# Kernel tuning notes

Measured on AMD Instinct MI355X. Metric: run time of the kernel, lower is better.

The kernel has to match this reference:

```python
import jax, jax.numpy as jnp
import numpy as np

N_NODES = 50000
BN_EPS = 1e-5


def setup_inputs() -> dict:
    key = jax.random.key(0)
    ks = jax.random.split(key, 6)
    N, E, CIN, CH, COUT = N_NODES, 800000, 128, 256, 128
    node_feat = jax.random.normal(ks[0], (N, CIN), dtype=jnp.float32)
    edge_index = jax.random.randint(ks[1], (2, E), 0, N, dtype=jnp.int64)
    # Glorot-ish init for weights
    W1 = jax.random.normal(ks[2], (CIN, CH), dtype=jnp.float32) / np.sqrt(CIN)
    b1 = jnp.zeros((CH,), dtype=jnp.float32)
    bn_gamma = jnp.ones((CH,), dtype=jnp.float32)
    bn_beta = jnp.zeros((CH,), dtype=jnp.float32)
    W2 = jax.random.normal(ks[3], (CH, COUT), dtype=jnp.float32) / np.sqrt(CH)
    b2 = jnp.zeros((COUT,), dtype=jnp.float32)
    return {"node_feat": node_feat, "edge_index": edge_index, "W1": W1, "b1": b1,
            "bn_gamma": bn_gamma, "bn_beta": bn_beta, "W2": W2, "b2": b2}


def gcn_conv(x, W, b, src, dst, n_nodes):
    """PyG GCNConv: out = D^-1/2 (A+I) D^-1/2 (x W) + b."""
    h = x @ W                                   # [N, C_out]
    loop = jnp.arange(n_nodes, dtype=src.dtype)
    src_f = jnp.concatenate([src, loop])        # self-loops appended
    dst_f = jnp.concatenate([dst, loop])
    deg = jax.ops.segment_sum(jnp.ones_like(dst_f, dtype=h.dtype), dst_f,
                              num_segments=n_nodes)
    dinv = jax.lax.rsqrt(jnp.maximum(deg, 1.0))  # deg >= 1 due to self-loops
    norm = dinv[src_f] * dinv[dst_f]             # [E+N]
    msg = h[src_f] * norm[:, None]               # gather + scale
    return jax.ops.segment_sum(msg, dst_f, num_segments=n_nodes) + b


def batch_norm(x, gamma, beta):
    mean = jnp.mean(x, axis=0)
    var = jnp.mean((x - mean) ** 2, axis=0)      # biased var (torch BN normalization)
    return (x - mean) * jax.lax.rsqrt(var + BN_EPS) * gamma + beta


def reference(node_feat, edge_index, W1, b1, bn_gamma, bn_beta, W2, b2):
    src, dst = edge_index[0], edge_index[1]
    x = gcn_conv(node_feat, W1, b1, src, dst, N_NODES)
    x = batch_norm(x, bn_gamma, bn_beta)
    x = jax.nn.relu(x)
    # dropout is identity at inference
    x = gcn_conv(x, W2, b2, src, dst, N_NODES)
    return x
```

## Files before the change

### kernel.cpp

```cpp
#include <hip/hip_runtime.h>
#include <hip/hip_fp16.h>

#define CIN 128
#define CH 256
#define COUT 128
#define BN_EPS 1e-5f

typedef __attribute__((ext_vector_type(8))) short bf16x8;
typedef __attribute__((ext_vector_type(4))) float f32x4;

__device__ __forceinline__ short f2bf(float x) {
    unsigned u = __float_as_uint(x);
    unsigned r = (u + 0x7fffu + ((u >> 16) & 1u)) >> 16;
    return (short)r;
}
__device__ __forceinline__ float bf2f(short h) {
    return __uint_as_float(((unsigned)(unsigned short)h) << 16);
}

__global__ void k_deg(const int* __restrict__ dst, int* __restrict__ degi,
                      unsigned short* __restrict__ rank, int E) {
    int e = blockIdx.x * 256 + threadIdx.x;
    if (e < E) rank[e] = (unsigned short)atomicAdd(&degi[dst[e]], 1);
}

__global__ void k_scan1(const int* __restrict__ degi, float* __restrict__ dinv,
                        int* __restrict__ blocksum, int N) {
    __shared__ int s[256];
    int i = blockIdx.x * 256 + threadIdx.x;
    int v = (i < N) ? degi[i] : 0;
    if (i < N) dinv[i] = rsqrtf((float)(v + 1));
    s[threadIdx.x] = v;
    __syncthreads();
    for (int st = 128; st > 0; st >>= 1) {
        if (threadIdx.x < st) s[threadIdx.x] += s[threadIdx.x + st];
        __syncthreads();
    }
    if (threadIdx.x == 0) blocksum[blockIdx.x] = s[0];
}

__global__ void k_scan3(const int* __restrict__ degi, const int* __restrict__ blocksum,
                        int nb, int* __restrict__ rowstart, int N, int E) {
    __shared__ int sb[256];
    __shared__ int s[256];
    int bv = (threadIdx.x < nb) ? blocksum[threadIdx.x] : 0;
    sb[threadIdx.x] = bv;
    __syncthreads();
    for (int st = 1; st < 256; st <<= 1) {
        int t = (threadIdx.x >= st) ? sb[threadIdx.x - st] : 0;
        __syncthreads();
        sb[threadIdx.x] += t;
        __syncthreads();
    }
    int boff = (blockIdx.x == 0) ? 0 : sb[blockIdx.x - 1];

    int i = blockIdx.x * 256 + threadIdx.x;
    int v = (i < N) ? degi[i] : 0;
    s[threadIdx.x] = v;
    __syncthreads();
    for (int st = 1; st < 256; st <<= 1) {
        int t = (threadIdx.x >= st) ? s[threadIdx.x - st] : 0;
        __syncthreads();
        s[threadIdx.x] += t;
        __syncthreads();
    }
    if (i < N) rowstart[i] = s[threadIdx.x] - v + boff;
    if (blockIdx.x == 0 && threadIdx.x == 0) rowstart[N] = E;
}

__global__ void k_fill(const int* __restrict__ src, const int* __restrict__ dst,
                       const unsigned short* __restrict__ rank,
                       const int* __restrict__ rowstart,
                       unsigned short* __restrict__ csr, int E) {
    int e = blockIdx.x * 256 + threadIdx.x;
    if (e >= E) return;
    int d = dst[e];
    int pos = rowstart[d] + (int)rank[e];
    __builtin_nontemporal_store((unsigned short)src[e], &csr[pos]);
}

__global__ void k_prep(const float* __restrict__ W1, const float* __restrict__ W2,
                       short* __restrict__ W1sw, short* __restrict__ W2sw,
                       const float4* __restrict__ nf, short4* __restrict__ nfb, int n4) {
    int t = blockIdx.x * 256 + threadIdx.x;
    if (t < 32768) {
        int n = t >> 7, kk = t & 127;
        float v = W1[kk * 256 + n];
        short h = f2bf(v);
        short l = f2bf(v - bf2f(h));
        int t16 = n >> 4, m = n & 15;
        int ks = kk >> 5, q = (kk >> 3) & 3, j = kk & 7;
        int idx = (t16 * 4 + ks) * 1024 + (q * 16 + m) * 8 + j;
        W1sw[idx] = h;
        W1sw[idx + 512] = l;
    } else if (t < 65536) {
        int u = t - 32768;
        int n = u >> 8, kk = u & 255;
        float v = W2[kk * 128 + n];
        short h = f2bf(v);
        short l = f2bf(v - bf2f(h));
        int t16 = n >> 4, m = n & 15;
        int ks = kk >> 5, q = (kk >> 3) & 3, j = kk & 7;
        int idx = (t16 * 8 + ks) * 1024 + (q * 16 + m) * 8 + j;
        W2sw[idx] = h;
        W2sw[idx + 512] = l;
    } else {
        int u = t - 65536;
        if (u < n4) {
            float4 v = nf[u];
            short4 s;
            s.x = f2bf(v.x); s.y = f2bf(v.y); s.z = f2bf(v.z); s.w = f2bf(v.w);
            nfb[u] = s;
        }
    }
}

template <int MODE>
__global__ __launch_bounds__(256) void k_gather(const short* __restrict__ xb,
                                                const int* __restrict__ rowstart,
                                                const unsigned short* __restrict__ csr,
                                                const float* __restrict__ dinv,
                                                const float* __restrict__ bias,
                                                float* __restrict__ out,
                                                short* __restrict__ ob, int N) {
    int t = blockIdx.x * 256 + threadIdx.x;
    int r = t >> 4;
    int c = t & 15;
    if (r >= N) return;
    float di = dinv[r];
    float w0 = di * di;
    bf16x8 sv = *(const bf16x8*)(xb + (size_t)r * 128 + c * 8);
    float acc[8];
    #pragma unroll
    for (int j = 0; j < 8; ++j) acc[j] = bf2f(sv[j]) * w0;
    int e0 = rowstart[r], e1 = rowstart[r + 1];
    int e = e0;
    for (; e + 7 < e1; e += 8) {
        int s[8];
        #pragma unroll
        for (int i = 0; i < 8; ++i) s[i] = csr[e + i];
        float w[8];
        #pragma unroll
        for (int i = 0; i < 8; ++i) w[i] = dinv[s[i]] * di;
        bf16x8 x[8];
        #pragma unroll
        for (int i = 0; i < 8; ++i) x[i] = *(const bf16x8*)(xb + (size_t)s[i] * 128 + c * 8);
        #pragma unroll
        for (int i = 0; i < 8; ++i)
            #pragma unroll
            for (int j = 0; j < 8; ++j) acc[j] = fmaf(w[i], bf2f(x[i][j]), acc[j]);
    }
    for (; e + 3 < e1; e += 4) {
        int s[4];
        #pragma unroll
        for (int i = 0; i < 4; ++i) s[i] = csr[e + i];
        float w[4];
        #pragma unroll
        for (int i = 0; i < 4; ++i) w[i] = dinv[s[i]] * di;
        bf16x8 x[4];
        #pragma unroll
        for (int i = 0; i < 4; ++i) x[i] = *(const bf16x8*)(xb + (size_t)s[i] * 128 + c * 8);
        #pragma unroll
        for (int i = 0; i < 4; ++i)
            #pragma unroll
            for (int j = 0; j < 8; ++j) acc[j] = fmaf(w[i], bf2f(x[i][j]), acc[j]);
    }
    for (; e < e1; ++e) {
        int s0 = csr[e];
        float ww = dinv[s0] * di;
        bf16x8 x0 = *(const bf16x8*)(xb + (size_t)s0 * 128 + c * 8);
        #pragma unroll
        for (int j = 0; j < 8; ++j) acc[j] = fmaf(ww, bf2f(x0[j]), acc[j]);
    }
    if (MODE == 0) {
        bf16x8 h;
        #pragma unroll
        for (int j = 0; j < 8; ++j) h[j] = f2bf(acc[j]);
        *(bf16x8*)(ob + (size_t)r * 128 + c * 8) = h;
    } else {
        float4 b0 = *(const float4*)(bias + c * 8);
        float4 b1 = *(const float4*)(bias + c * 8 + 4);
        float4 o0 = make_float4(acc[0] + b0.x, acc[1] + b0.y, acc[2] + b0.z, acc[3] + b0.w);
        float4 o1 = make_float4(acc[4] + b1.x, acc[5] + b1.y, acc[6] + b1.z, acc[7] + b1.w);
        *(float4*)(out + (size_t)r * 128 + c * 8) = o0;
        *(float4*)(out + (size_t)r * 128 + c * 8 + 4) = o1;
    }
}

__device__ __forceinline__ bf16x8 bnrelu8(bf16x8 raw, const float* __restrict__ scsh, int c) {
    float4 sc0 = *(const float4*)(scsh + c);
    float4 sc1 = *(const float4*)(scsh + c + 4);
    float4 sh0 = *(const float4*)(scsh + 256 + c);
    float4 sh1 = *(const float4*)(scsh + 256 + c + 4);
    bf16x8 o;
    o[0] = f2bf(fmaxf(fmaf(bf2f(raw[0]), sc0.x, sh0.x), 0.f));
    o[1] = f2bf(fmaxf(fmaf(bf2f(raw[1]), sc0.y, sh0.y), 0.f));
    o[2] = f2bf(fmaxf(fmaf(bf2f(raw[2]), sc0.z, sh0.z), 0.f));
    o[3] = f2bf(fmaxf(fmaf(bf2f(raw[3]), sc0.w, sh0.w), 0.f));
    o[4] = f2bf(fmaxf(fmaf(bf2f(raw[4]), sc1.x, sh1.x), 0.f));
    o[5] = f2bf(fmaxf(fmaf(bf2f(raw[5]), sc1.y, sh1.y), 0.f));
    o[6] = f2bf(fmaxf(fmaf(bf2f(raw[6]), sc1.z, sh1.z), 0.f));
    o[7] = f2bf(fmaxf(fmaf(bf2f(raw[7]), sc1.w, sh1.w), 0.f));
    return o;
}

template <int K, int NOUT, bool STATS, bool BIAS, bool BNRELU>
__global__ __launch_bounds__(256, 2) void k_gemm(const short* __restrict__ A,
                                                 const short* __restrict__ Bsw,
                                                 const float* __restrict__ bias,
                                                 const float* __restrict__ scsh,
                                                 short* __restrict__ C,
                                                 float* __restrict__ stats, int M) {
    constexpr int CT = NOUT / 64;
    constexpr int KS = K / 32;
    constexpr int KP = K + 8;
    constexpr int LROW = NOUT + 8;
    constexpr int LSZ = (64 * KP > 64 * LROW) ? 64 * KP : 64 * LROW;
    __shared__ __align__(16) short lds[LSZ];
    int tid = threadIdx.x;
    int wave = tid >> 6;
    int lane = tid & 63;
    int m = lane & 15;
    int q = lane >> 4;
    int row0 = blockIdx.x * 64;

    constexpr int CPRA = K / 8;
    #pragma unroll
    for (int i = 0; i < (64 * CPRA) / 256; ++i) {
        int idx = i * 256 + tid;
        int r = idx / CPRA, cc = idx % CPRA;
        int gr = row0 + r;
        if (gr >= M) gr = M - 1;
        bf16x8 v = *(const bf16x8*)(A + (size_t)gr * K + cc * 8);
        if (BNRELU) v = bnrelu8(v, scsh, cc * 8);
        *(bf16x8*)(lds + r * KP + cc * 8) = v;
    }
    __syncthreads();

    f32x4 acc[4][CT];
    #pragma unroll
    for (int rt = 0; rt < 4; ++rt)
        #pragma unroll
        for (int ct = 0; ct < CT; ++ct)
            acc[rt][ct] = (f32x4){0.f, 0.f, 0.f, 0.f};

    #pragma unroll
    for (int ks = 0; ks < KS; ++ks) {
        bf16x8 bh[CT], bl[CT];
        #pragma unroll
        for (int ct = 0; ct < CT; ++ct) {
            const short* bp = Bsw + (size_t)((wave * CT + ct) * KS + ks) * 1024 + lane * 8;
            bh[ct] = *(const bf16x8*)bp;
            bl[ct] = *(const bf16x8*)(bp + 512);
        }
        bf16x8 af[4];
        #pragma unroll
        for (int rt = 0; rt < 4; ++rt)
            af[rt] = *(const bf16x8*)(lds + (rt * 16 + m) * KP + ks * 32 + q * 8);
        #pragma unroll
        for (int ct = 0; ct < CT; ++ct)
            #pragma unroll
            for (int rt = 0; rt < 4; ++rt) {
                acc[rt][ct] = __builtin_amdgcn_mfma_f32_16x16x32_bf16(af[rt], bh[ct], acc[rt][ct], 0, 0, 0);
                acc[rt][ct] = __builtin_amdgcn_mfma_f32_16x16x32_bf16(af[rt], bl[ct], acc[rt][ct], 0, 0, 0);
            }
    }
    __syncthreads();

    #pragma unroll
    for (int ct = 0; ct < CT; ++ct) {
        int col = wave * (NOUT / 4) + ct * 16 + m;
        float bv = BIAS ? bias[col] : 0.f;
        float s = 0.f, sq = 0.f;
        #pragma unroll
        for (int rt = 0; rt < 4; ++rt) {
            #pragma unroll
            for (int r = 0; r < 4; ++r) {
                int lrow = rt * 16 + q * 4 + r;
                float v = acc[rt][ct][r] + bv;
                if (STATS && row0 + lrow < M) { s += v; sq = fmaf(v, v, sq); }
                lds[lrow * LROW + col] = f2bf(v);
            }
        }
        if (STATS) {
            s += __shfl_xor(s, 16, 64);
            s += __shfl_xor(s, 32, 64);
            sq += __shfl_xor(sq, 16, 64);
            sq += __shfl_xor(sq, 32, 64);
            if (lane < 16) {
                unsafeAtomicAdd(&stats[col], s);
                unsafeAtomicAdd(&stats[256 + col], sq);
            }
        }
    }
    __syncthreads();
    constexpr int CPR = NOUT / 8;
    #pragma unroll
    for (int i = 0; i < (64 * CPR) / 256; ++i) {
        int idx = i * 256 + tid;
        int row = idx / CPR;
        int ch = idx % CPR;
        if (row0 + row < M)
            *(bf16x8*)(C + (size_t)(row0 + row) * NOUT + ch * 8) =
                *(const bf16x8*)(lds + row * LROW + ch * 8);
    }
}

__global__ void k_bnfinal(const float* __restrict__ stats, const float* __restrict__ gamma,
                          const float* __restrict__ beta, float* __restrict__ scsh, int N) {
    int c = threadIdx.x;
    float invN = 1.0f / (float)N;
    float mean = stats[c] * invN;
    float var = stats[256 + c] * invN - mean * mean;
    var = fmaxf(var, 0.f);
    float inv = rsqrtf(var + BN_EPS);
    float sc = gamma[c] * inv;
    scsh[c] = sc;
    scsh[256 + c] = fmaf(-mean, sc, beta[c]);
}

extern "C" void kernel_launch(void* const* d_in, const int* in_sizes, int n_in,
                              void* d_out, int out_size, void* d_ws, size_t ws_size,
                              hipStream_t stream) {
    const float* nf    = (const float*)d_in[0];
    const int*   ei    = (const int*)d_in[1];
    const float* W1    = (const float*)d_in[2];
    const float* b1    = (const float*)d_in[3];
    const float* gamma = (const float*)d_in[4];
    const float* beta  = (const float*)d_in[5];
    const float* W2    = (const float*)d_in[6];
    const float* b2    = (const float*)d_in[7];
    float* out = (float*)d_out;

    const int N = in_sizes[0] / CIN;
    const int E = in_sizes[1] / 2;
    const int* src = ei;
    const int* dst = ei + E;

    char* ws = (char*)d_ws;
    auto align256 = [](size_t x) { return (x + 255) & ~(size_t)255; };
    size_t off = 0;
    int*   degi = (int*)(ws + off);      off += align256((size_t)N * 4);
    float* stats = (float*)(ws + off);   off += align256(512 * 4);
    size_t zspan = off;
    float* dinv = (float*)(ws + off);    off += align256((size_t)N * 4);
    int*   rowstart = (int*)(ws + off);  off += align256((size_t)(N + 1) * 4);
    int*   blocksum = (int*)(ws + off);  off += align256(256 * 4);
    float* scsh = (float*)(ws + off);    off += align256(512 * 4);
    short* W1sw = (short*)(ws + off);    off += align256(65536 * 2);
    short* W2sw = (short*)(ws + off);    off += align256(65536 * 2);
    unsigned short* rank = (unsigned short*)(ws + off); off += align256((size_t)E * 2);
    unsigned short* csr = (unsigned short*)(ws + off);  off += align256((size_t)E * 2);
    short* nfb = (short*)(ws + off);     off += align256((size_t)N * CIN * 2);
    short* agg1b = (short*)(ws + off);   off += align256((size_t)N * CIN * 2);
    short* x1b = (short*)(ws + off);     off += align256((size_t)N * CH * 2);
    short* yb = (short*)(ws + off);      off += align256((size_t)N * COUT * 2);

    int nbN = (N + 255) / 256;
    int nbE = (E + 255) / 256;
    int n4 = N * 32;

    hipMemsetAsync(ws, 0, zspan, stream);

    k_prep<<<(65536 + n4 + 255) / 256, 256, 0, stream>>>(
        W1, W2, W1sw, W2sw, (const float4*)nf, (short4*)nfb, n4);

    k_deg<<<nbE, 256, 0, stream>>>(dst, degi, rank, E);
    k_scan1<<<nbN, 256, 0, stream>>>(degi, dinv, blocksum, N);
    k_scan3<<<nbN, 256, 0, stream>>>(degi, blocksum, nbN, rowstart, N, E);
    k_fill<<<nbE, 256, 0, stream>>>(src, dst, rank, rowstart, csr, E);

    k_gather<0><<<(N * 16 + 255) / 256, 256, 0, stream>>>(
        nfb, rowstart, csr, dinv, nullptr, nullptr, agg1b, N);

    k_gemm<CIN, CH, true, true, false><<<(N + 63) / 64, 256, 0, stream>>>(
        agg1b, W1sw, b1, nullptr, x1b, stats, N);

    k_bnfinal<<<1, 256, 0, stream>>>(stats, gamma, beta, scsh, N);

    k_gemm<CH, COUT, false, false, true><<<(N + 63) / 64, 256, 0, stream>>>(
        x1b, W2sw, nullptr, scsh, yb, nullptr, N);

    k_gather<1><<<(N * 16 + 255) / 256, 256, 0, stream>>>(
        yb, rowstart, csr, dinv, b2, out, nullptr, N);
}
```

Baseline: 276.9 us.

## Replace BN stats atomics with per-block partials and double-buffer B-fragment loads

The first GEMM now writes per-block column sums and sums of squares to a partials buffer instead of doing global float atomics. A new small kernel reduces those partials with 8 blocks before the BN finalize step. The GEMM inner loop also double-buffers the B-fragment register loads, prefetching the next k-step while MFMAs run on the current one. This is meant to cut atomic contention and hide global-load latency, at the cost of an extra kernel launch, more registers and more workspace traffic.

```diff
diff --git a/kernel.cpp b/kernel.cpp
--- a/kernel.cpp
+++ b/kernel.cpp
@@ -210,7 +210,7 @@
                                                  const float* __restrict__ bias,
                                                  const float* __restrict__ scsh,
                                                  short* __restrict__ C,
-                                                 float* __restrict__ stats, int M) {
+                                                 float* __restrict__ partials, int M) {
     constexpr int CT = NOUT / 64;
     constexpr int KS = K / 32;
     constexpr int KP = K + 8;
@@ -244,14 +244,24 @@
         for (int ct = 0; ct < CT; ++ct)
             acc[rt][ct] = (f32x4){0.f, 0.f, 0.f, 0.f};
 
+    bf16x8 bh[2][CT], bl[2][CT];
+    #pragma unroll
+    for (int ct = 0; ct < CT; ++ct) {
+        const short* bp = Bsw + (size_t)((wave * CT + ct) * KS) * 1024 + lane * 8;
+        bh[0][ct] = *(const bf16x8*)bp;
+        bl[0][ct] = *(const bf16x8*)(bp + 512);
+    }
+
     #pragma unroll
     for (int ks = 0; ks < KS; ++ks) {
-        bf16x8 bh[CT], bl[CT];
-        #pragma unroll
-        for (int ct = 0; ct < CT; ++ct) {
-            const short* bp = Bsw + (size_t)((wave * CT + ct) * KS + ks) * 1024 + lane * 8;
-            bh[ct] = *(const bf16x8*)bp;
-            bl[ct] = *(const bf16x8*)(bp + 512);
+        const int cur = ks & 1, nxt = cur ^ 1;
+        if (ks + 1 < KS) {
+            #pragma unroll
+            for (int ct = 0; ct < CT; ++ct) {
+                const short* bp = Bsw + (size_t)((wave * CT + ct) * KS + ks + 1) * 1024 + lane * 8;
+                bh[nxt][ct] = *(const bf16x8*)bp;
+                bl[nxt][ct] = *(const bf16x8*)(bp + 512);
+            }
         }
         bf16x8 af[4];
         #pragma unroll
@@ -261,8 +271,8 @@
         for (int ct = 0; ct < CT; ++ct)
             #pragma unroll
             for (int rt = 0; rt < 4; ++rt) {
-                acc[rt][ct] = __builtin_amdgcn_mfma_f32_16x16x32_bf16(af[rt], bh[ct], acc[rt][ct], 0, 0, 0);
-                acc[rt][ct] = __builtin_amdgcn_mfma_f32_16x16x32_bf16(af[rt], bl[ct], acc[rt][ct], 0, 0, 0);
+                acc[rt][ct] = __builtin_amdgcn_mfma_f32_16x16x32_bf16(af[rt], bh[cur][ct], acc[rt][ct], 0, 0, 0);
+                acc[rt][ct] = __builtin_amdgcn_mfma_f32_16x16x32_bf16(af[rt], bl[cur][ct], acc[rt][ct], 0, 0, 0);
             }
     }
     __syncthreads();
@@ -288,8 +298,8 @@
             sq += __shfl_xor(sq, 16, 64);
             sq += __shfl_xor(sq, 32, 64);
             if (lane < 16) {
-                unsafeAtomicAdd(&stats[col], s);
-                unsafeAtomicAdd(&stats[256 + col], sq);
+                partials[(size_t)blockIdx.x * 512 + col] = s;
+                partials[(size_t)blockIdx.x * 512 + 256 + col] = sq;
             }
         }
     }
@@ -304,6 +314,17 @@
             *(bf16x8*)(C + (size_t)(row0 + row) * NOUT + ch * 8) =
                 *(const bf16x8*)(lds + row * LROW + ch * 8);
     }
+}
+
+__global__ void k_redstats(const float* __restrict__ partials, float* __restrict__ stats,
+                           int nb, int rpb) {
+    int sid = threadIdx.x;
+    int r0 = blockIdx.x * rpb;
+    int r1 = r0 + rpb;
+    if (r1 > nb) r1 = nb;
+    float acc = 0.f;
+    for (int r = r0; r < r1; ++r) acc += partials[(size_t)r * 512 + sid];
+    unsafeAtomicAdd(&stats[sid], acc);
 }
 
 __global__ void k_bnfinal(const float* __restrict__ stats, const float* __restrict__ gamma,
@@ -337,6 +358,8 @@
     const int* src = ei;
     const int* dst = ei + E;
 
+    const int nb1 = (N + 63) / 64;
+
     char* ws = (char*)d_ws;
     auto align256 = [](size_t x) { return (x + 255) & ~(size_t)255; };
     size_t off = 0;
@@ -349,6 +372,7 @@
     float* scsh = (float*)(ws + off);    off += align256(512 * 4);
     short* W1sw = (short*)(ws + off);    off += align256(65536 * 2);
     short* W2sw = (short*)(ws + off);    off += align256(65536 * 2);
+    float* partials = (float*)(ws + off); off += align256((size_t)nb1 * 512 * 4);
     unsigned short* rank = (unsigned short*)(ws + off); off += align256((size_t)E * 2);
     unsigned short* csr = (unsigned short*)(ws + off);  off += align256((size_t)E * 2);
     short* nfb = (short*)(ws + off);     off += align256((size_t)N * CIN * 2);
@@ -373,12 +397,17 @@
     k_gather<0><<<(N * 16 + 255) / 256, 256, 0, stream>>>(
         nfb, rowstart, csr, dinv, nullptr, nullptr, agg1b, N);
 
-    k_gemm<CIN, CH, true, true, false><<<(N + 63) / 64, 256, 0, stream>>>(
-        agg1b, W1sw, b1, nullptr, x1b, stats, N);
-
+    k_gemm<CIN, CH, true, true, false><<<nb1, 256, 0, stream>>>(
+        agg1b, W1sw, b1, nullptr, x1b, partials, N);
+
+    {
+        int rblocks = 8;
+        int rpb = (nb1 + rblocks - 1) / rblocks;
+        k_redstats<<<rblocks, 512, 0, stream>>>(partials, stats, nb1, rpb);
+    }
     k_bnfinal<<<1, 256, 0, stream>>>(stats, gamma, beta, scsh, N);
 
-    k_gemm<CH, COUT, false, false, true><<<(N + 63) / 64, 256, 0, stream>>>(
+    k_gemm<CH, COUT, false, false, true><<<nb1, 256, 0, stream>>>(
         x1b, W2sw, nullptr, scsh, yb, nullptr, N);
 
     k_gather<1><<<(N * 16 + 255) / 256, 256, 0, stream>>>(
```

Result: no change. 277.5 us (+0.2%).
